# Kernel tuning notes

Measured on AMD Instinct MI355X. Metric: run time of the kernel, lower is better.

## Reference

```python
import jax, jax.numpy as jnp
import numpy as np
from jax import lax

B = 8192
DEPTH = 4096
SCALES = 3
FLT = 4  # db2 filter length

_DB2_DEC_LO = np.array([-0.12940952255092145, 0.22414386804185735, 0.836516303737469, 0.48296291314469025], dtype=np.float32)
_DB2_DEC_HI = np.array([-0.48296291314469025, 0.836516303737469, 0.22414386804185735, 0.12940952255092145], dtype=np.float32)


def _coeff_lens(depth, flen, scales):
    # mirrors pywt.dwt_coeff_len(n, flen, 'zero') = floor((n + flen - 1) / 2)
    lens = [depth]
    for _ in range(scales):
        lens.append((lens[-1] + flen - 1) // 2)
    lens = lens[1:]
    lens.append(lens[-1])
    return lens  # e.g. [2049, 1026, 514, 514]

WAVE_DEPTH = int(np.sum(_coeff_lens(DEPTH, FLT, SCALES)))  # 4103


def setup_inputs() -> dict:
    key = jax.random.key(0)
    ks = jax.random.split(key, 5)
    x = jax.random.normal(ks[0], (B, DEPTH), dtype=jnp.float32)
    diag_b = 1.0 + 0.1 * jax.random.normal(ks[1], (DEPTH,), dtype=jnp.float32)
    diag_g = 1.0 + 0.1 * jax.random.normal(ks[2], (WAVE_DEPTH,), dtype=jnp.float32)
    diag_s = 1.0 + 0.1 * jax.random.normal(ks[3], (DEPTH,), dtype=jnp.float32)
    dec_lo = jnp.asarray(_DB2_DEC_LO)
    dec_hi = jnp.asarray(_DB2_DEC_HI)
    rec_lo = dec_lo[::-1]
    rec_hi = dec_hi[::-1]
    perm_idx = jax.random.permutation(ks[4], WAVE_DEPTH).astype(jnp.int32)
    return {"x": x, "diag_b": diag_b, "diag_g": diag_g, "diag_s": diag_s,
            "dec_lo": dec_lo, "dec_hi": dec_hi, "rec_lo": rec_lo, "rec_hi": rec_hi,
            "perm_idx": perm_idx}


def _forward(x, diag_b, diag_g, diag_s, dec_lo, dec_hi, rec_lo, rec_hi, perm_idx):
    L = dec_lo.shape[0]
    lens = _coeff_lens(x.shape[-1], L, SCALES)
    # mul_b: diag(vec) matmul == elementwise column scale
    a = x * diag_b
    # multi-level analysis DWT with 'zero' padding: full convolution, keep odd indices
    w_dec = jnp.stack([dec_lo[::-1], dec_hi[::-1]])[:, None, :]  # [2,1,L] (flip: lax does corr)
    details = []
    for _ in range(SCALES):
        y = lax.conv_general_dilated(a[:, None, :], w_dec, (2,), [(L - 2, L - 1)],
                                     dimension_numbers=("NCH", "OIH", "NCH"))
        a, d = y[:, 0, :], y[:, 1, :]
        details.append(d)
    c = jnp.concatenate([a] + details[::-1], axis=-1)  # [B, WAVE_DEPTH], [cA_s, cD_s, ..., cD_1]
    # mul_p: permutation matmul == column gather
    c = c[:, perm_idx]
    # mul_g
    c = c * diag_g
    # coefficient slicing exactly as in the original forward (incl. its start-update rule)
    rev = lens[::-1]
    coeffs = []
    start = 0
    for s_i in range(SCALES + 1):
        stop = start + rev[s_i]
        coeffs.append(c[:, start:stop])
        start = lens[s_i]
    # multi-level reconstruction (idwt, zero mode): zero-upsample, full conv, trim L-2 per side
    a = coeffs[0]
    w_rec = jnp.stack([rec_lo[::-1], rec_hi[::-1]])[None, :, :]  # [1,2,L]
    for d in coeffs[1:]:
        if a.shape[-1] == d.shape[-1] + 1:  # pywt waverec odd-length trim
            a = a[:, :-1]
        xin = jnp.stack([a, d], axis=1)  # [B,2,la]
        a = lax.conv_general_dilated(xin, w_rec, (1,), [(1, 1)], lhs_dilation=(2,),
                                     dimension_numbers=("NCH", "OIH", "NCH"))[:, 0, :]
    # mul_s
    return a * diag_s


def reference(x, diag_b, diag_g, diag_s, dec_lo, dec_hi, rec_lo, rec_hi, perm_idx):
    return _forward(x, diag_b, diag_g, diag_s, dec_lo, dec_hi, rec_lo, rec_hi, perm_idx)
```

## Files before the change

kernel.cpp:

```cpp
#include <hip/hip_runtime.h>


#define NT 512

__global__ __launch_bounds__(NT, 8) void wavelet_fused(
    const float* __restrict__ x,
    const float* __restrict__ diag_b,
    const float* __restrict__ diag_g,
    const float* __restrict__ diag_s,
    const float* __restrict__ dec_lo,
    const float* __restrict__ dec_hi,
    const float* __restrict__ rec_lo,
    const float* __restrict__ rec_hi,
    const int*   __restrict__ perm_idx,
    float* __restrict__ out)
{
    __shared__ __align__(16) float rawA[4 + 4112];
    __shared__ __align__(16) float rawC[4 + 4112];
    float* const A = rawA + 4;
    float* const C = rawC + 4;

    const int tid = threadIdx.x;
    const long row = blockIdx.x;

    const float lo0=dec_lo[0], lo1=dec_lo[1], lo2=dec_lo[2], lo3=dec_lo[3];
    const float hi0=dec_hi[0], hi1=dec_hi[1], hi2=dec_hi[2], hi3=dec_hi[3];
    const float rl0=rec_lo[0], rl1=rec_lo[1], rl2=rec_lo[2], rl3=rec_lo[3];
    const float rh0=rec_hi[0], rh1=rec_hi[1], rh2=rec_hi[2], rh3=rec_hi[3];

    {
        const float4* xr = (const float4*)(x + row * 4096);
        const float4* bb = (const float4*)diag_b;
        float4* A4 = (float4*)A;
        for (int i = tid; i < 1024; i += NT) {
            float4 v = xr[i], w = bb[i];
            v.x *= w.x; v.y *= w.y; v.z *= w.z; v.w *= w.w;
            A4[i] = v;
        }
        if (tid < 4)  rawA[tid] = 0.0f;
        if (tid < 8)  A[4096 + tid] = 0.0f;
        if (tid < 4)  rawC[tid] = 0.0f;
        if (tid < 11) C[2049 + tid] = 0.0f;
    }
    __syncthreads();

    for (int n = tid; n < 2049; n += NT) {
        float2 u0 = *(const float2*)(A + 2*n - 2);
        float2 u1 = *(const float2*)(A + 2*n);
        C[n]        = lo0*u1.y + lo1*u1.x + lo2*u0.y + lo3*u0.x;
        C[2060 + n] = hi0*u1.y + hi1*u1.x + hi2*u0.y + hi3*u0.x;
    }
    __syncthreads();

    if (tid < 6) A[1026 + tid] = 0.0f;
    for (int n = tid; n < 1026; n += NT) {
        float2 u0 = *(const float2*)(C + 2*n - 2);
        float2 u1 = *(const float2*)(C + 2*n);
        A[n]        = lo0*u1.y + lo1*u1.x + lo2*u0.y + lo3*u0.x;
        A[1032 + n] = hi0*u1.y + hi1*u1.x + hi2*u0.y + hi3*u0.x;
    }
    __syncthreads();

    for (int n = tid; n < 514; n += NT) {
        float2 u0 = *(const float2*)(A + 2*n - 2);
        float2 u1 = *(const float2*)(A + 2*n);
        C[n]       = lo0*u1.y + lo1*u1.x + lo2*u0.y + lo3*u0.x;
        C[514 + n] = hi0*u1.y + hi1*u1.x + hi2*u0.y + hi3*u0.x;
    }
    for (int j = tid; j < 513; j += NT) {
        *(float2*)(C + 1028 + 2*j) = *(const float2*)(A + 1032 + 2*j);
    }
    __syncthreads();

    for (int q = tid; q < 1025; q += NT) {
        int4  pj = ((const int4*)perm_idx)[q];
        float4 g4 = ((const float4*)diag_g)[q];
        float4 v;
        v.x = C[pj.x + (pj.x >= 2054 ? 6 : 0)] * g4.x;
        v.y = C[pj.y + (pj.y >= 2054 ? 6 : 0)] * g4.y;
        v.z = C[pj.z + (pj.z >= 2054 ? 6 : 0)] * g4.z;
        v.w = C[pj.w + (pj.w >= 2054 ? 6 : 0)] * g4.w;
        ((float4*)A)[q] = v;
    }
    if (tid < 3) {
        int i = 4100 + tid;
        int j = perm_idx[i];
        A[i] = C[j + (j >= 2054 ? 6 : 0)] * diag_g[i];
    }
    __syncthreads();

    for (int u = tid; u < 257; u += NT) {
        int p0 = 2 * u;
        float a0v = A[p0],        a1v = A[p0 + 1],    a2v = A[p0 + 2];
        float d0v = A[2049 + p0], d1v = A[2050 + p0], d2v = A[2051 + p0];
        float4 w;
        w.x = rl2*a0v + rl0*a1v + rh2*d0v + rh0*d1v;
        w.y = rl3*a0v + rl1*a1v + rh3*d0v + rh1*d1v;
        w.z = rl2*a1v + rl0*a2v + rh2*d1v + rh0*d2v;
        w.w = rl3*a1v + rl1*a2v + rh3*d1v + rh1*d2v;
        if (u < 256) *(float4*)(C + 4*u) = w;
        else         { C[4*u] = w.x; C[4*u + 1] = w.y; }
    }
    __syncthreads();

    for (int u = tid; u < 513; u += NT) {
        int p0 = 2 * u;
        float a0v = C[p0], a1v = C[p0 + 1], a2v = C[p0 + 2];
        float2 dd = *(const float2*)(A + 1026 + p0);
        float d2v = A[1028 + p0];
        float4 w;
        w.x = rl2*a0v + rl0*a1v + rh2*dd.x + rh0*dd.y;
        w.y = rl3*a0v + rl1*a1v + rh3*dd.x + rh1*dd.y;
        w.z = rl2*a1v + rl0*a2v + rh2*dd.y + rh0*d2v;
        w.w = rl3*a1v + rl1*a2v + rh3*dd.y + rh1*d2v;
        if (u < 512) *(float4*)(C + 1028 + 4*u) = w;
        else         { C[1028 + 4*u] = w.x; C[1028 + 4*u + 1] = w.y; }
    }
    __syncthreads();

    {
        const float4* ss = (const float4*)diag_s;
        float4* outr = (float4*)(out + row * 4096);
        for (int u = tid; u < 512; u += NT) {
            int b = 1028 + 4 * u;
            float4 aa = *(const float4*)(C + b);
            float a4v = C[b + 4];
            float2 dd0 = *(const float2*)(A + 514 + 4*u);
            float2 dd1 = *(const float2*)(A + 516 + 4*u);
            float d4v  = A[518 + 4*u];
            float4 s0 = ss[2*u], s1 = ss[2*u + 1];
            float4 o0, o1;
            o0.x = (rl2*aa.x + rl0*aa.y + rh2*dd0.x + rh0*dd0.y) * s0.x;
            o0.y = (rl3*aa.x + rl1*aa.y + rh3*dd0.x + rh1*dd0.y) * s0.y;
            o0.z = (rl2*aa.y + rl0*aa.z + rh2*dd0.y + rh0*dd1.x) * s0.z;
            o0.w = (rl3*aa.y + rl1*aa.z + rh3*dd0.y + rh1*dd1.x) * s0.w;
            o1.x = (rl2*aa.z + rl0*aa.w + rh2*dd1.x + rh0*dd1.y) * s1.x;
            o1.y = (rl3*aa.z + rl1*aa.w + rh3*dd1.x + rh1*dd1.y) * s1.y;
            o1.z = (rl2*aa.w + rl0*a4v  + rh2*dd1.y + rh0*d4v ) * s1.z;
            o1.w = (rl3*aa.w + rl1*a4v  + rh3*dd1.y + rh1*d4v ) * s1.w;
            outr[2*u]     = o0;
            outr[2*u + 1] = o1;
        }
    }
}

extern "C" void kernel_launch(void* const* d_in, const int* in_sizes, int n_in,
                              void* d_out, int out_size, void* d_ws, size_t ws_size,
                              hipStream_t stream) {
    const float* x       = (const float*)d_in[0];
    const float* diag_b  = (const float*)d_in[1];
    const float* diag_g  = (const float*)d_in[2];
    const float* diag_s  = (const float*)d_in[3];
    const float* dec_lo  = (const float*)d_in[4];
    const float* dec_hi  = (const float*)d_in[5];
    const float* rec_lo  = (const float*)d_in[6];
    const float* rec_hi  = (const float*)d_in[7];
    const int*   perm    = (const int*)d_in[8];
    float* out = (float*)d_out;

    const int B = in_sizes[0] / 4096;
    wavelet_fused<<<B, NT, 0, stream>>>(
        x, diag_b, diag_g, diag_s, dec_lo, dec_hi, rec_lo, rec_hi, perm, out);
}
```

Before: 256.9 us.

## Fuse first DWT level into load and gather permutation inline during reconstruction

Computes the first analysis level directly from registers while loading x, removing the staging write of the scaled input to LDS. The separate permuted-coefficient buffer is dropped: reconstruction stages gather coefficients through perm_idx and diag_g on the fly. This removes two barriers and a full LDS pass and shrinks shared memory, which may raise occupancy. The cost is redundant global reads of perm_idx and diag_g in the gather stages, and the kernel now hardcodes one thread per 8 input elements (NT=512).

```diff
diff --git a/kernel.cpp b/kernel.cpp
--- a/kernel.cpp
+++ b/kernel.cpp
@@ -15,10 +15,12 @@
     const int*   __restrict__ perm_idx,
     float* __restrict__ out)
 {
-    __shared__ __align__(16) float rawA[4 + 4112];
-    __shared__ __align__(16) float rawC[4 + 4112];
-    float* const A = rawA + 4;
-    float* const C = rawC + 4;
+    __shared__ __align__(16) float rawA[3088];
+    __shared__ __align__(16) float rawC[4112];
+    float* const A1 = rawA + 4;
+    float* const A2 = rawA + 2060;
+    float* const R1 = rawA + 4;
+    float* const Cc = rawC;
 
     const int tid = threadIdx.x;
     const long row = blockIdx.x;
@@ -28,119 +30,125 @@
     const float rl0=rec_lo[0], rl1=rec_lo[1], rl2=rec_lo[2], rl3=rec_lo[3];
     const float rh0=rec_hi[0], rh1=rec_hi[1], rh2=rec_hi[2], rh3=rec_hi[3];
 
+    if (tid < 2) rawA[2 + tid]    = 0.0f;
+    if (tid < 3) rawA[2053 + tid] = 0.0f;
+    if (tid < 2) rawA[2058 + tid] = 0.0f;
+    if (tid < 2) rawA[3086 + tid] = 0.0f;
+
     {
-        const float4* xr = (const float4*)(x + row * 4096);
-        const float4* bb = (const float4*)diag_b;
-        float4* A4 = (float4*)A;
-        for (int i = tid; i < 1024; i += NT) {
-            float4 v = xr[i], w = bb[i];
-            v.x *= w.x; v.y *= w.y; v.z *= w.z; v.w *= w.w;
-            A4[i] = v;
+        const float* xr = x + row * 4096;
+        float4 xv0 = *(const float4*)(xr + 8*tid);
+        float4 xv1 = *(const float4*)(xr + 8*tid + 4);
+        float4 bv0 = *(const float4*)(diag_b + 8*tid);
+        float4 bv1 = *(const float4*)(diag_b + 8*tid + 4);
+        float vm2 = 0.0f, vm1 = 0.0f;
+        if (tid > 0) {
+            float2 xm = *(const float2*)(xr + 8*tid - 2);
+            float2 bm = *(const float2*)(diag_b + 8*tid - 2);
+            vm2 = xm.x * bm.x; vm1 = xm.y * bm.y;
         }
-        if (tid < 4)  rawA[tid] = 0.0f;
-        if (tid < 8)  A[4096 + tid] = 0.0f;
-        if (tid < 4)  rawC[tid] = 0.0f;
-        if (tid < 11) C[2049 + tid] = 0.0f;
+        float v0 = xv0.x*bv0.x, v1 = xv0.y*bv0.y, v2 = xv0.z*bv0.z, v3 = xv0.w*bv0.w;
+        float v4 = xv1.x*bv1.x, v5 = xv1.y*bv1.y, v6 = xv1.z*bv1.z, v7 = xv1.w*bv1.w;
+        float4 av, dv;
+        av.x = lo0*v1 + lo1*v0 + lo2*vm1 + lo3*vm2;
+        dv.x = hi0*v1 + hi1*v0 + hi2*vm1 + hi3*vm2;
+        av.y = lo0*v3 + lo1*v2 + lo2*v1 + lo3*v0;
+        dv.y = hi0*v3 + hi1*v2 + hi2*v1 + hi3*v0;
+        av.z = lo0*v5 + lo1*v4 + lo2*v3 + lo3*v2;
+        dv.z = hi0*v5 + hi1*v4 + hi2*v3 + hi3*v2;
+        av.w = lo0*v7 + lo1*v6 + lo2*v5 + lo3*v4;
+        dv.w = hi0*v7 + hi1*v6 + hi2*v5 + hi3*v4;
+        *(float4*)(A1 + 4*tid) = av;
+        *(float4*)(Cc + 2056 + 4*tid) = dv;
+        if (tid == 0) {
+            float xa = xr[4094]*diag_b[4094], xb = xr[4095]*diag_b[4095];
+            A1[2048]        = lo2*xb + lo3*xa;
+            Cc[2056 + 2048] = hi2*xb + hi3*xa;
+        }
     }
     __syncthreads();
 
-    for (int n = tid; n < 2049; n += NT) {
-        float2 u0 = *(const float2*)(A + 2*n - 2);
-        float2 u1 = *(const float2*)(A + 2*n);
-        C[n]        = lo0*u1.y + lo1*u1.x + lo2*u0.y + lo3*u0.x;
-        C[2060 + n] = hi0*u1.y + hi1*u1.x + hi2*u0.y + hi3*u0.x;
+    for (int p = tid; p < 513; p += NT) {
+        float2 u0 = *(const float2*)(A1 + 4*p - 2);
+        float4 u1 = *(const float4*)(A1 + 4*p);
+        float2 ap, dp;
+        ap.x = lo0*u1.y + lo1*u1.x + lo2*u0.y + lo3*u0.x;
+        dp.x = hi0*u1.y + hi1*u1.x + hi2*u0.y + hi3*u0.x;
+        ap.y = lo0*u1.w + lo1*u1.z + lo2*u1.y + lo3*u1.x;
+        dp.y = hi0*u1.w + hi1*u1.z + hi2*u1.y + hi3*u1.x;
+        *(float2*)(A2 + 2*p)        = ap;
+        *(float2*)(Cc + 1028 + 2*p) = dp;
     }
     __syncthreads();
 
-    if (tid < 6) A[1026 + tid] = 0.0f;
-    for (int n = tid; n < 1026; n += NT) {
-        float2 u0 = *(const float2*)(C + 2*n - 2);
-        float2 u1 = *(const float2*)(C + 2*n);
-        A[n]        = lo0*u1.y + lo1*u1.x + lo2*u0.y + lo3*u0.x;
-        A[1032 + n] = hi0*u1.y + hi1*u1.x + hi2*u0.y + hi3*u0.x;
+    for (int p = tid; p < 257; p += NT) {
+        float2 u0 = *(const float2*)(A2 + 4*p - 2);
+        float4 u1 = *(const float4*)(A2 + 4*p);
+        float2 ap, dp;
+        ap.x = lo0*u1.y + lo1*u1.x + lo2*u0.y + lo3*u0.x;
+        dp.x = hi0*u1.y + hi1*u1.x + hi2*u0.y + hi3*u0.x;
+        ap.y = lo0*u1.w + lo1*u1.z + lo2*u1.y + lo3*u1.x;
+        dp.y = hi0*u1.w + hi1*u1.z + hi2*u1.y + hi3*u1.x;
+        *(float2*)(Cc + 2*p)       = ap;
+        *(float2*)(Cc + 514 + 2*p) = dp;
     }
     __syncthreads();
 
-    for (int n = tid; n < 514; n += NT) {
-        float2 u0 = *(const float2*)(A + 2*n - 2);
-        float2 u1 = *(const float2*)(A + 2*n);
-        C[n]       = lo0*u1.y + lo1*u1.x + lo2*u0.y + lo3*u0.x;
-        C[514 + n] = hi0*u1.y + hi1*u1.x + hi2*u0.y + hi3*u0.x;
-    }
-    for (int j = tid; j < 513; j += NT) {
-        *(float2*)(C + 1028 + 2*j) = *(const float2*)(A + 1032 + 2*j);
-    }
-    __syncthreads();
+    auto CPj = [&](int j) -> float {
+        return Cc[j + (j >= 2054 ? 2 : 0)];
+    };
+    auto CP = [&](int i) -> float {
+        return CPj(perm_idx[i]) * diag_g[i];
+    };
 
-    for (int q = tid; q < 1025; q += NT) {
-        int4  pj = ((const int4*)perm_idx)[q];
-        float4 g4 = ((const float4*)diag_g)[q];
-        float4 v;
-        v.x = C[pj.x + (pj.x >= 2054 ? 6 : 0)] * g4.x;
-        v.y = C[pj.y + (pj.y >= 2054 ? 6 : 0)] * g4.y;
-        v.z = C[pj.z + (pj.z >= 2054 ? 6 : 0)] * g4.z;
-        v.w = C[pj.w + (pj.w >= 2054 ? 6 : 0)] * g4.w;
-        ((float4*)A)[q] = v;
-    }
-    if (tid < 3) {
-        int i = 4100 + tid;
-        int j = perm_idx[i];
-        A[i] = C[j + (j >= 2054 ? 6 : 0)] * diag_g[i];
-    }
-    __syncthreads();
-
-    for (int u = tid; u < 257; u += NT) {
-        int p0 = 2 * u;
-        float a0v = A[p0],        a1v = A[p0 + 1],    a2v = A[p0 + 2];
-        float d0v = A[2049 + p0], d1v = A[2050 + p0], d2v = A[2051 + p0];
-        float4 w;
-        w.x = rl2*a0v + rl0*a1v + rh2*d0v + rh0*d1v;
-        w.y = rl3*a0v + rl1*a1v + rh3*d0v + rh1*d1v;
-        w.z = rl2*a1v + rl0*a2v + rh2*d1v + rh0*d2v;
-        w.w = rl3*a1v + rl1*a2v + rh3*d1v + rh1*d2v;
-        if (u < 256) *(float4*)(C + 4*u) = w;
-        else         { C[4*u] = w.x; C[4*u + 1] = w.y; }
-    }
-    __syncthreads();
-
-    for (int u = tid; u < 513; u += NT) {
-        int p0 = 2 * u;
-        float a0v = C[p0], a1v = C[p0 + 1], a2v = C[p0 + 2];
-        float2 dd = *(const float2*)(A + 1026 + p0);
-        float d2v = A[1028 + p0];
-        float4 w;
-        w.x = rl2*a0v + rl0*a1v + rh2*dd.x + rh0*dd.y;
-        w.y = rl3*a0v + rl1*a1v + rh3*dd.x + rh1*dd.y;
-        w.z = rl2*a1v + rl0*a2v + rh2*dd.y + rh0*d2v;
-        w.w = rl3*a1v + rl1*a2v + rh3*dd.y + rh1*d2v;
-        if (u < 512) *(float4*)(C + 1028 + 4*u) = w;
-        else         { C[1028 + 4*u] = w.x; C[1028 + 4*u + 1] = w.y; }
+    for (int k = tid; k < 513; k += NT) {
+        float a0 = CP(k),        a1v = CP(k + 1);
+        float d0 = CP(2049 + k), d1v = CP(2050 + k);
+        float2 w;
+        w.x = rl2*a0 + rl0*a1v + rh2*d0 + rh0*d1v;
+        w.y = rl3*a0 + rl1*a1v + rh3*d0 + rh1*d1v;
+        *(float2*)(R1 + 2*k) = w;
     }
     __syncthreads();
 
     {
-        const float4* ss = (const float4*)diag_s;
+        const int u = tid;
+        float2 q01 = *(const float2*)(R1 + 2*u);
+        float2 q23 = *(const float2*)(R1 + 2*u + 2);
+        int2   pe0 = *(const int2*)(perm_idx + 1026 + 2*u);
+        int2   pe1 = *(const int2*)(perm_idx + 1028 + 2*u);
+        float2 ge0 = *(const float2*)(diag_g + 1026 + 2*u);
+        float2 ge1 = *(const float2*)(diag_g + 1028 + 2*u);
+        float e0 = CPj(pe0.x) * ge0.x, e1 = CPj(pe0.y) * ge0.y;
+        float e2 = CPj(pe1.x) * ge1.x, e3 = CPj(pe1.y) * ge1.y;
+        float s0  = rl2*q01.x + rl0*q01.y + rh2*e0 + rh0*e1;
+        float s1v = rl3*q01.x + rl1*q01.y + rh3*e0 + rh1*e1;
+        float s2v = rl2*q01.y + rl0*q23.x + rh2*e1 + rh0*e2;
+        float s3v = rl3*q01.y + rl1*q23.x + rh3*e1 + rh1*e2;
+        float s4  = rl2*q23.x + rl0*q23.y + rh2*e2 + rh0*e3;
+        int2   pf0 = *(const int2*)(perm_idx + 514 + 4*u);
+        int2   pf1 = *(const int2*)(perm_idx + 516 + 4*u);
+        int    pf2 = perm_idx[518 + 4*u];
+        float2 gf0 = *(const float2*)(diag_g + 514 + 4*u);
+        float2 gf1 = *(const float2*)(diag_g + 516 + 4*u);
+        float  gf2 = diag_g[518 + 4*u];
+        float f0 = CPj(pf0.x) * gf0.x, f1 = CPj(pf0.y) * gf0.y;
+        float f2 = CPj(pf1.x) * gf1.x, f3 = CPj(pf1.y) * gf1.y;
+        float f4 = CPj(pf2)   * gf2;
+        float4 ss0 = ((const float4*)diag_s)[2*u];
+        float4 ss1 = ((const float4*)diag_s)[2*u + 1];
+        float4 o0, o1;
+        o0.x = (rl2*s0  + rl0*s1v + rh2*f0 + rh0*f1) * ss0.x;
+        o0.y = (rl3*s0  + rl1*s1v + rh3*f0 + rh1*f1) * ss0.y;
+        o0.z = (rl2*s1v + rl0*s2v + rh2*f1 + rh0*f2) * ss0.z;
+        o0.w = (rl3*s1v + rl1*s2v + rh3*f1 + rh1*f2) * ss0.w;
+        o1.x = (rl2*s2v + rl0*s3v + rh2*f2 + rh0*f3) * ss1.x;
+        o1.y = (rl3*s2v + rl1*s3v + rh3*f2 + rh1*f3) * ss1.y;
+        o1.z = (rl2*s3v + rl0*s4  + rh2*f3 + rh0*f4) * ss1.z;
+        o1.w = (rl3*s3v + rl1*s4  + rh3*f3 + rh1*f4) * ss1.w;
         float4* outr = (float4*)(out + row * 4096);
-        for (int u = tid; u < 512; u += NT) {
-            int b = 1028 + 4 * u;
-            float4 aa = *(const float4*)(C + b);
-            float a4v = C[b + 4];
-            float2 dd0 = *(const float2*)(A + 514 + 4*u);
-            float2 dd1 = *(const float2*)(A + 516 + 4*u);
-            float d4v  = A[518 + 4*u];
-            float4 s0 = ss[2*u], s1 = ss[2*u + 1];
-            float4 o0, o1;
-            o0.x = (rl2*aa.x + rl0*aa.y + rh2*dd0.x + rh0*dd0.y) * s0.x;
-            o0.y = (rl3*aa.x + rl1*aa.y + rh3*dd0.x + rh1*dd0.y) * s0.y;
-            o0.z = (rl2*aa.y + rl0*aa.z + rh2*dd0.y + rh0*dd1.x) * s0.z;
-            o0.w = (rl3*aa.y + rl1*aa.z + rh3*dd0.y + rh1*dd1.x) * s0.w;
-            o1.x = (rl2*aa.z + rl0*aa.w + rh2*dd1.x + rh0*dd1.y) * s1.x;
-            o1.y = (rl3*aa.z + rl1*aa.w + rh3*dd1.x + rh1*dd1.y) * s1.y;
-            o1.z = (rl2*aa.w + rl0*a4v  + rh2*dd1.y + rh0*d4v ) * s1.z;
-            o1.w = (rl3*aa.w + rl1*a4v  + rh3*dd1.y + rh1*d4v ) * s1.w;
-            outr[2*u]     = o0;
-            outr[2*u + 1] = o1;
-        }
+        outr[2*u]     = o0;
+        outr[2*u + 1] = o1;
     }
 }
 
```

Measured after the change: 269.5 us. +4.9%, slower.
